# Kernel optimization log

Hardware: AMD Instinct MI355X
Metric: run time of the kernel (lower is better)

## Reference

```python
import jax, jax.numpy as jnp
import numpy as np

HIDDEN = 128
N_NODES = 50000
N_EDGES = 600000
EPS = 1e-5


def setup_inputs() -> dict:
    key = jax.random.key(0)
    ks = jax.random.split(key, 10)
    x = jax.random.normal(ks[0], (N_NODES, HIDDEN), dtype=jnp.float32)
    edge_index = jax.random.randint(ks[1], (2, N_EDGES), 0, N_NODES, dtype=jnp.int64)
    edge_type = jax.random.randint(ks[2], (N_EDGES,), 0, 3, dtype=jnp.int64)
    s = 0.02
    # Stacked per-type message weights: [3, 2H, H] (types 0=power, 1=comm, 2=cross)
    Wmsg = jax.random.normal(ks[3], (3, 2 * HIDDEN, HIDDEN), dtype=jnp.float32) * s
    bmsg = jnp.zeros((3, HIDDEN), dtype=jnp.float32)
    Wupd = jax.random.normal(ks[4], (2 * HIDDEN, HIDDEN), dtype=jnp.float32) * s
    bupd = jnp.zeros((HIDDEN,), dtype=jnp.float32)
    gamma = jnp.ones((HIDDEN,), dtype=jnp.float32)
    beta = jnp.zeros((HIDDEN,), dtype=jnp.float32)
    return {
        "x": x, "edge_index": edge_index, "edge_type": edge_type,
        "Wmsg": Wmsg, "bmsg": bmsg, "Wupd": Wupd, "bupd": bupd,
        "gamma": gamma, "beta": beta,
    }


def reference(x, edge_index, edge_type, Wmsg, bmsg, Wupd, bupd, gamma, beta):
    src, dst = edge_index[0], edge_index[1]
    N = x.shape[0]
    E = edge_type.shape[0]
    # Typed-edge gather + linear message: [E, 2H]
    msg_input = jnp.concatenate([x[src], x[dst]], axis=-1)
    # Compute all 3 typed linears, then select per-edge type: [E, 3, H] -> [E, H]
    all_msgs = jnp.einsum('ec,tch->eth', msg_input, Wmsg) + bmsg
    messages = jnp.take_along_axis(all_msgs, edge_type[:, None, None], axis=1)[:, 0]
    # scatter_add aggregation + count-normalize (count clamped to >= 1)
    agg = jax.ops.segment_sum(messages, dst, num_segments=N)
    count = jax.ops.segment_sum(jnp.ones((E, 1), dtype=x.dtype), dst, num_segments=N)
    agg = agg / jnp.maximum(count, 1.0)
    # Update MLP: Linear -> LayerNorm -> GELU (Dropout is identity in eval)
    h = jnp.concatenate([x, agg], axis=-1) @ Wupd + bupd
    mu = jnp.mean(h, axis=-1, keepdims=True)
    var = jnp.var(h, axis=-1, keepdims=True)
    hn = (h - mu) / jnp.sqrt(var + EPS) * gamma + beta
    x_updated = jax.nn.gelu(hn, approximate=False)
    return x + x_updated
```

## Files before the change

### kernel.cpp

```cpp
#include <hip/hip_runtime.h>
#include <hip/hip_bf16.h>
#include <math.h>

#define HIDDEN 128
#define NNODES 50000
#define NEDGES 600000
#define EPS 1e-5f
#define SCAN_CHUNK 1024
#define NSCAN_BLOCKS ((NNODES + SCAN_CHUNK - 1) / SCAN_CHUNK)
#define MPAD 50048

#define P0_W6T_END   384
#define P0_BV_END    387
#define P0_WUT_END   515
#define P0_XB_END    (515 + 6256)
#define P0_HIST_END  (P0_XB_END + 2344)

#define OFF_W6T  ((size_t)0)
#define OFF_BV   ((size_t)196608)
#define OFF_WUT  ((size_t)199680)
#define OFF_XB   ((size_t)265216)
#define OFF_ABB  ((size_t)13077504)
#define OFF_AGB  ((size_t)51477504)
#define OFF_HIST ((size_t)64289792)
#define OFF_EXCL ((size_t)64489984)
#define OFF_CURS ((size_t)64690176)
#define OFF_BSUM ((size_t)64890368)
#define OFF_PACK ((size_t)64890624)

typedef __attribute__((ext_vector_type(8))) short bf16x8;
typedef __attribute__((ext_vector_type(4))) float f32x4;

__device__ inline unsigned short f2bf(float f) {
    union { float f; unsigned u; } c; c.f = f;
    unsigned u = c.u;
    u += 0x7FFF + ((u >> 16) & 1);
    return (unsigned short)(u >> 16);
}
__device__ inline float bf2f(unsigned short h) {
    union { unsigned u; float f; } c; c.u = ((unsigned)h) << 16;
    return c.f;
}

__device__ inline unsigned char f2fp8(float f) {
    int d = __builtin_amdgcn_cvt_pk_fp8_f32(f, f, 0, false);
    return (unsigned char)(d & 0xFF);
}
template <int S>
__device__ inline float fp8f(unsigned q) {
    return __builtin_amdgcn_cvt_f32_fp8(q, S);
}

__global__ __launch_bounds__(256) void phase0(const float* __restrict__ Wmsg,
                                              const float* __restrict__ bmsg,
                                              const float* __restrict__ Wupd,
                                              const float* __restrict__ x,
                                              const int* __restrict__ ei,
                                              unsigned short* __restrict__ W6T,
                                              float* __restrict__ Bv,
                                              unsigned short* __restrict__ WuT,
                                              unsigned short* __restrict__ Xb,
                                              int* __restrict__ hist) {
    const int b = blockIdx.x;
    const int tid = threadIdx.x;
    if (b < P0_W6T_END) {
        int idx = b * 256 + tid;
        int col = idx >> 7;
        int k = idx & 127;
        int half = col >= 384;
        int rem = col - half * 384;
        int t = rem >> 7;
        int h = rem & 127;
        W6T[idx] = f2bf(Wmsg[t * 32768 + (half * 128 + k) * 128 + h]);
    } else if (b < P0_BV_END) {
        int idx = (b - P0_W6T_END) * 256 + tid;
        if (idx < 768) Bv[idx] = (idx < 384) ? 0.f : bmsg[idx - 384];
    } else if (b < P0_WUT_END) {
        int idx = (b - P0_BV_END) * 256 + tid;
        int n = idx >> 8;
        int k = idx & 255;
        WuT[idx] = f2bf(Wupd[(size_t)k * 128 + n]);
    } else if (b < P0_XB_END) {
        int i = (b - P0_WUT_END) * 256 + tid;
        int base = i * 4;
        if (base < MPAD * 128) {
            ushort4 o;
            if (base < NNODES * 128) {
                float4 v = *(const float4*)(x + base);
                o.x = f2bf(v.x); o.y = f2bf(v.y); o.z = f2bf(v.z); o.w = f2bf(v.w);
            } else {
                o.x = o.y = o.z = o.w = 0;
            }
            *(ushort4*)(Xb + base) = o;
        }
    } else {
        int e = (b - P0_XB_END) * 256 + tid;
        if (e < NEDGES) atomicAdd(&hist[ei[NEDGES + e]], 1);
    }
}

__global__ __launch_bounds__(256) void gemm_ab(const unsigned short* __restrict__ Xb,
                                               const unsigned short* __restrict__ W6T,
                                               const float* __restrict__ Bv,
                                               unsigned char* __restrict__ ABb8) {
    __shared__ unsigned char lds_buf[64 * 272];
    const int tid = threadIdx.x;
    const int mbase = blockIdx.x * 64;
    const int w = tid >> 6;
    const int nbase = blockIdx.y * 256 + w * 64;
    const int lane = tid & 63;
    const int r = lane & 15;
    const int quad = lane >> 4;

    bf16x8 b[4][4];
#pragma unroll
    for (int ks = 0; ks < 4; ++ks)
#pragma unroll
        for (int ni = 0; ni < 4; ++ni)
            b[ks][ni] = *(const bf16x8*)(W6T + (size_t)(nbase + ni * 16 + r) * 128 + ks * 32 + quad * 8);

    unsigned short* xs = (unsigned short*)lds_buf;
#pragma unroll
    for (int i = 0; i < 4; ++i) {
        int item = i * 256 + tid;
        int row = item >> 4;
        int kb = item & 15;
        bf16x8 v = *(const bf16x8*)(Xb + (size_t)(mbase + row) * 128 + kb * 8);
        *(bf16x8*)&xs[row * 128 + ((kb ^ (row & 7)) * 8)] = v;
    }
    __syncthreads();

    f32x4 acc[4][4];
#pragma unroll
    for (int mi = 0; mi < 4; ++mi)
#pragma unroll
        for (int ni = 0; ni < 4; ++ni) acc[mi][ni] = (f32x4){0.f, 0.f, 0.f, 0.f};

#pragma unroll
    for (int ks = 0; ks < 4; ++ks) {
        bf16x8 a[4];
        const int kb = ks * 4 + quad;
#pragma unroll
        for (int mi = 0; mi < 4; ++mi)
            a[mi] = *(const bf16x8*)&xs[(mi * 16 + r) * 128 + ((kb ^ (r & 7)) * 8)];
#pragma unroll
        for (int mi = 0; mi < 4; ++mi)
#pragma unroll
            for (int ni = 0; ni < 4; ++ni)
                acc[mi][ni] = __builtin_amdgcn_mfma_f32_16x16x32_bf16(a[mi], b[ks][ni], acc[mi][ni], 0, 0, 0);
    }

    __syncthreads();
    unsigned char (*tile)[272] = (unsigned char(*)[272])lds_buf;

#pragma unroll
    for (int ni = 0; ni < 4; ++ni) {
        const int col_l = w * 64 + ni * 16 + r;
        const float bias = Bv[blockIdx.y * 256 + col_l];
#pragma unroll
        for (int mi = 0; mi < 4; ++mi) {
            f32x4 v = acc[mi][ni];
#pragma unroll
            for (int reg = 0; reg < 4; ++reg) {
                tile[mi * 16 + quad * 4 + reg][col_l] = f2fp8(v[reg] + bias);
            }
        }
    }
    __syncthreads();

#pragma unroll
    for (int i = 0; i < 4; ++i) {
        int item = i * 256 + tid;
        int row_l = item >> 4;
        int chunk = item & 15;
        int grow = mbase + row_l;
        if (grow < NNODES) {
            uint4 v = *(const uint4*)&tile[row_l][chunk * 16];
            *(uint4*)(ABb8 + (size_t)grow * 768 + blockIdx.y * 256 + chunk * 16) = v;
        }
    }
}

__global__ __launch_bounds__(256) void scan_phase1(const int* __restrict__ hist,
                                                   int* __restrict__ excl,
                                                   int* __restrict__ blockSums) {
    __shared__ int lds[256];
    const int blk = blockIdx.x;
    const int t = threadIdx.x;
    const int base = blk * SCAN_CHUNK + t * 4;
    int v[4];
    int s = 0;
#pragma unroll
    for (int i = 0; i < 4; ++i) {
        v[i] = (base + i < NNODES) ? hist[base + i] : 0;
        s += v[i];
    }
    lds[t] = s;
    __syncthreads();
    for (int off = 1; off < 256; off <<= 1) {
        int add = (t >= off) ? lds[t - off] : 0;
        __syncthreads();
        lds[t] += add;
        __syncthreads();
    }
    int incl = lds[t];
    int run = incl - s;
#pragma unroll
    for (int i = 0; i < 4; ++i) {
        if (base + i < NNODES) excl[base + i] = run;
        run += v[i];
    }
    if (t == 255) blockSums[blk] = incl;
}

__global__ __launch_bounds__(256) void scan_phase3(int* __restrict__ excl,
                                                   const int* __restrict__ blockSums,
                                                   int* __restrict__ cursor) {
    __shared__ int s_add;
    const int blk = blockIdx.x;
    const int t = threadIdx.x;
    if (t < 64) {
        int v = (t < blk) ? blockSums[t] : 0;
#pragma unroll
        for (int off = 32; off >= 1; off >>= 1) v += __shfl_xor(v, off, 64);
        if (t == 0) s_add = v;
    }
    __syncthreads();
    const int add = s_add;
    for (int i = t; i < SCAN_CHUNK; i += 256) {
        int idx = blk * SCAN_CHUNK + i;
        if (idx < NNODES) {
            int o = excl[idx] + add;
            excl[idx] = o;
            cursor[idx] = o;
        }
    }
}

__global__ __launch_bounds__(256) void edge_bucket(const int* __restrict__ ei,
                                                   const int* __restrict__ et,
                                                   int* __restrict__ cursor,
                                                   unsigned* __restrict__ packed) {
    int e = blockIdx.x * 256 + threadIdx.x;
    if (e >= NEDGES) return;
    int src = ei[e];
    int dst = ei[NEDGES + e];
    int t = et[e];
    int pos = atomicAdd(&cursor[dst], 1);
    packed[pos] = (unsigned)(src * 192 + t * 32) | ((unsigned)t << 25);
}

__global__ __launch_bounds__(256) void aggregate(const unsigned* __restrict__ packed,
                                                 const int* __restrict__ excl,
                                                 const int* __restrict__ hist,
                                                 const unsigned char* __restrict__ ABb8,
                                                 unsigned short* __restrict__ Agb) {
    const int n = blockIdx.x * 4 + (threadIdx.x >> 6);
    const int lane = threadIdx.x & 63;
    if (n >= NNODES) return;
    const int start = excl[n];
    const int deg = hist[n];
    const unsigned* ABu = (const unsigned*)ABb8;

    const int half = lane >> 5;
    const int cl = lane & 31;

    float s0 = 0.f, s1 = 0.f, s2 = 0.f, s3 = 0.f;
    int c1 = 0, c2 = 0;

    for (int base = 0; base < deg; base += 64) {
        const int m = min(64, deg - base);
        unsigned v = 0;
        if (lane < m) v = packed[start + base + lane];
        int j = 0;
        for (; j + 8 <= m; j += 8) {
            unsigned e0 = __shfl(v, j + 0 + half, 64);
            unsigned e1 = __shfl(v, j + 2 + half, 64);
            unsigned e2 = __shfl(v, j + 4 + half, 64);
            unsigned e3 = __shfl(v, j + 6 + half, 64);
            unsigned q0 = ABu[(e0 & 0x1FFFFFF) + cl];
            unsigned q1 = ABu[(e1 & 0x1FFFFFF) + cl];
            unsigned q2 = ABu[(e2 & 0x1FFFFFF) + cl];
            unsigned q3 = ABu[(e3 & 0x1FFFFFF) + cl];
            int t0 = e0 >> 25, t1 = e1 >> 25, t2 = e2 >> 25, t3 = e3 >> 25;
            c1 += (t0 == 1) + (t1 == 1) + (t2 == 1) + (t3 == 1);
            c2 += (t0 == 2) + (t1 == 2) + (t2 == 2) + (t3 == 2);
            s0 += (fp8f<0>(q0) + fp8f<0>(q1)) + (fp8f<0>(q2) + fp8f<0>(q3));
            s1 += (fp8f<1>(q0) + fp8f<1>(q1)) + (fp8f<1>(q2) + fp8f<1>(q3));
            s2 += (fp8f<2>(q0) + fp8f<2>(q1)) + (fp8f<2>(q2) + fp8f<2>(q3));
            s3 += (fp8f<3>(q0) + fp8f<3>(q1)) + (fp8f<3>(q2) + fp8f<3>(q3));
        }
        for (; j + 2 <= m; j += 2) {
            unsigned e0 = __shfl(v, j + half, 64);
            unsigned q0 = ABu[(e0 & 0x1FFFFFF) + cl];
            int t0 = e0 >> 25;
            c1 += (t0 == 1);
            c2 += (t0 == 2);
            s0 += fp8f<0>(q0); s1 += fp8f<1>(q0);
            s2 += fp8f<2>(q0); s3 += fp8f<3>(q0);
        }
        if (j < m) {
            unsigned e0 = __shfl(v, j, 64);
            if (half == 0) {
                unsigned q0 = ABu[(e0 & 0x1FFFFFF) + cl];
                int t0 = e0 >> 25;
                c1 += (t0 == 1);
                c2 += (t0 == 2);
                s0 += fp8f<0>(q0); s1 += fp8f<1>(q0);
                s2 += fp8f<2>(q0); s3 += fp8f<3>(q0);
            }
        }
    }

    s0 += __shfl_xor(s0, 32, 64);
    s1 += __shfl_xor(s1, 32, 64);
    s2 += __shfl_xor(s2, 32, 64);
    s3 += __shfl_xor(s3, 32, 64);
    c1 += __shfl_xor(c1, 32, 64);
    c2 += __shfl_xor(c2, 32, 64);
    const int c0 = deg - c1 - c2;

    const unsigned* brow = ABu + (size_t)n * 192 + 96;
    if (c0) {
        unsigned p = brow[cl];
        s0 += c0 * fp8f<0>(p); s1 += c0 * fp8f<1>(p);
        s2 += c0 * fp8f<2>(p); s3 += c0 * fp8f<3>(p);
    }
    if (c1) {
        unsigned p = brow[32 + cl];
        s0 += c1 * fp8f<0>(p); s1 += c1 * fp8f<1>(p);
        s2 += c1 * fp8f<2>(p); s3 += c1 * fp8f<3>(p);
    }
    if (c2) {
        unsigned p = brow[64 + cl];
        s0 += c2 * fp8f<0>(p); s1 += c2 * fp8f<1>(p);
        s2 += c2 * fp8f<2>(p); s3 += c2 * fp8f<3>(p);
    }

    const float inv = 1.0f / fmaxf((float)deg, 1.0f);
    if (half == 0) {
        uint2 o;
        o.x = (unsigned)f2bf(s0 * inv) | ((unsigned)f2bf(s1 * inv) << 16);
        o.y = (unsigned)f2bf(s2 * inv) | ((unsigned)f2bf(s3 * inv) << 16);
        ((uint2*)(Agb + (size_t)n * 128))[cl] = o;
    }
}

__global__ __launch_bounds__(256, 4) void update_mfma(const unsigned short* __restrict__ Xb,
                                                      const unsigned short* __restrict__ Agb,
                                                      const unsigned short* __restrict__ WuT,
                                                      const float* __restrict__ bupd,
                                                      const float* __restrict__ gamma,
                                                      const float* __restrict__ beta,
                                                      float* __restrict__ out) {
    const int tid = threadIdx.x;
    const int rowbase = blockIdx.x * 64 + (tid >> 6) * 16;
    const int lane = tid & 63;
    const int r = lane & 15;
    const int quad = lane >> 4;

    bf16x8 a[8];
#pragma unroll
    for (int ks = 0; ks < 4; ++ks)
        a[ks] = *(const bf16x8*)(Xb + (size_t)(rowbase + r) * 128 + ks * 32 + quad * 8);
#pragma unroll
    for (int ks = 4; ks < 8; ++ks)
        a[ks] = *(const bf16x8*)(Agb + (size_t)(rowbase + r) * 128 + (ks - 4) * 32 + quad * 8);

    bf16x8 e0, e1;
    const int tgt0 = r;
    const int tgt1 = 16 + r;
#pragma unroll
    for (int t = 0; t < 8; ++t) {
        e0[t] = (short)((quad * 8 + t == tgt0) ? 0x3F80 : 0);
        e1[t] = (short)((quad * 8 + t == tgt1) ? 0x3F80 : 0);
    }
    f32x4 xr[8];
#pragma unroll
    for (int ni = 0; ni < 8; ++ni) {
        f32x4 z = (f32x4){0.f, 0.f, 0.f, 0.f};
        xr[ni] = __builtin_amdgcn_mfma_f32_16x16x32_bf16(a[ni >> 1], (ni & 1) ? e1 : e0, z, 0, 0, 0);
    }

    f32x4 acc[8];
#pragma unroll
    for (int ni = 0; ni < 8; ++ni) acc[ni] = (f32x4){0.f, 0.f, 0.f, 0.f};

#pragma unroll
    for (int ks = 0; ks < 8; ++ks) {
        const int kb = ks * 4 + quad;
#pragma unroll
        for (int ni = 0; ni < 8; ++ni) {
            bf16x8 b = *(const bf16x8*)(WuT + (size_t)(ni * 16 + r) * 256 + kb * 8);
            acc[ni] = __builtin_amdgcn_mfma_f32_16x16x32_bf16(a[ks], b, acc[ni], 0, 0, 0);
        }
    }

    float vals[8][4];
    float gcol[8], bcol[8];
#pragma unroll
    for (int ni = 0; ni < 8; ++ni) {
        const int col = ni * 16 + r;
        const float bias = bupd[col];
        gcol[ni] = gamma[col];
        bcol[ni] = beta[col];
#pragma unroll
        for (int reg = 0; reg < 4; ++reg) vals[ni][reg] = acc[ni][reg] + bias;
    }

#pragma unroll
    for (int reg = 0; reg < 4; ++reg) {
        float s = 0.f, s2 = 0.f;
#pragma unroll
        for (int ni = 0; ni < 8; ++ni) {
            s += vals[ni][reg];
            s2 += vals[ni][reg] * vals[ni][reg];
        }
#pragma unroll
        for (int off = 8; off >= 1; off >>= 1) {
            s += __shfl_xor(s, off, 64);
            s2 += __shfl_xor(s2, off, 64);
        }
        const int row = rowbase + quad * 4 + reg;
        if (row < NNODES) {
            const float mu = s * (1.0f / 128.0f);
            const float var = s2 * (1.0f / 128.0f) - mu * mu;
            const float inv = rsqrtf(var + EPS);
#pragma unroll
            for (int ni = 0; ni < 8; ++ni) {
                const int col = ni * 16 + r;
                float hn = (vals[ni][reg] - mu) * inv * gcol[ni] + bcol[ni];
                float ge = 0.5f * hn * (1.0f + erff(hn * 0.70710678118654752f));
                out[(size_t)row * 128 + col] = xr[ni][reg] + ge;
            }
        }
    }
}

extern "C" void kernel_launch(void* const* d_in, const int* in_sizes, int n_in,
                              void* d_out, int out_size, void* d_ws, size_t ws_size,
                              hipStream_t stream) {
    const float* x     = (const float*)d_in[0];
    const int*   ei    = (const int*)d_in[1];
    const int*   et    = (const int*)d_in[2];
    const float* Wmsg  = (const float*)d_in[3];
    const float* bmsg  = (const float*)d_in[4];
    const float* Wupd  = (const float*)d_in[5];
    const float* bupd  = (const float*)d_in[6];
    const float* gamma = (const float*)d_in[7];
    const float* beta  = (const float*)d_in[8];
    float* out = (float*)d_out;

    char* ws = (char*)d_ws;
    unsigned short* W6T  = (unsigned short*)(ws + OFF_W6T);
    float*          Bv   = (float*)(ws + OFF_BV);
    unsigned short* WuT  = (unsigned short*)(ws + OFF_WUT);
    unsigned short* Xb   = (unsigned short*)(ws + OFF_XB);
    unsigned char*  ABb8 = (unsigned char*)(ws + OFF_ABB);
    unsigned short* Agb  = (unsigned short*)(ws + OFF_AGB);
    int*            hist = (int*)(ws + OFF_HIST);
    int*            excl = (int*)(ws + OFF_EXCL);
    int*            curs = (int*)(ws + OFF_CURS);
    int*            bsum = (int*)(ws + OFF_BSUM);
    unsigned*       pack = (unsigned*)(ws + OFF_PACK);

    (void)hipMemsetAsync(hist, 0, NNODES * sizeof(int), stream);

    phase0<<<P0_HIST_END, 256, 0, stream>>>(Wmsg, bmsg, Wupd, x, ei, W6T, Bv, WuT, Xb, hist);
    gemm_ab<<<dim3(MPAD / 64, 3), 256, 0, stream>>>(Xb, W6T, Bv, ABb8);
    scan_phase1<<<NSCAN_BLOCKS, 256, 0, stream>>>(hist, excl, bsum);
    scan_phase3<<<NSCAN_BLOCKS, 256, 0, stream>>>(excl, bsum, curs);
    edge_bucket<<<(NEDGES + 255) / 256, 256, 0, stream>>>(ei, et, curs, pack);
    aggregate<<<(NNODES + 3) / 4, 256, 0, stream>>>(pack, excl, hist, ABb8, Agb);
    update_mfma<<<MPAD / 64, 256, 0, stream>>>(Xb, Agb, WuT, bupd, gamma, beta, out);
}
```

Measured before the change: 260.6 us.

## Split update GEMM output columns across two waves with shared-memory LayerNorm reduction

The update kernel now gives each 16-row tile to two wavefronts, each computing half of the 128 output columns. LayerNorm sum and sum-of-squares partials are combined through shared memory behind a block barrier. Blocks cover 32 rows instead of 64, so the grid doubles, and launch bounds are raised to allow more resident blocks. This cuts per-wave accumulator registers and serial MFMA chains to raise occupancy. The cost is a __syncthreads, duplicate A-fragment loads across the wave pair, and more blocks.

```diff
diff --git a/kernel.cpp b/kernel.cpp
--- a/kernel.cpp
+++ b/kernel.cpp
@@ -346,18 +346,24 @@
     }
 }
 
-__global__ __launch_bounds__(256, 4) void update_mfma(const unsigned short* __restrict__ Xb,
+__global__ __launch_bounds__(256, 5) void update_mfma(const unsigned short* __restrict__ Xb,
                                                       const unsigned short* __restrict__ Agb,
                                                       const unsigned short* __restrict__ WuT,
                                                       const float* __restrict__ bupd,
                                                       const float* __restrict__ gamma,
                                                       const float* __restrict__ beta,
                                                       float* __restrict__ out) {
+    __shared__ float sred[2][2][32];
+
     const int tid = threadIdx.x;
-    const int rowbase = blockIdx.x * 64 + (tid >> 6) * 16;
+    const int w = tid >> 6;
+    const int wrow = w >> 1;
+    const int whalf = w & 1;
     const int lane = tid & 63;
     const int r = lane & 15;
     const int quad = lane >> 4;
+    const int rowbase = blockIdx.x * 32 + wrow * 16;
+    const int nibase = whalf * 4;
 
     bf16x8 a[8];
 #pragma unroll
@@ -368,70 +374,82 @@
         a[ks] = *(const bf16x8*)(Agb + (size_t)(rowbase + r) * 128 + (ks - 4) * 32 + quad * 8);
 
     bf16x8 e0, e1;
-    const int tgt0 = r;
-    const int tgt1 = 16 + r;
 #pragma unroll
     for (int t = 0; t < 8; ++t) {
-        e0[t] = (short)((quad * 8 + t == tgt0) ? 0x3F80 : 0);
-        e1[t] = (short)((quad * 8 + t == tgt1) ? 0x3F80 : 0);
-    }
-    f32x4 xr[8];
-#pragma unroll
-    for (int ni = 0; ni < 8; ++ni) {
+        e0[t] = (short)((quad * 8 + t == r) ? 0x3F80 : 0);
+        e1[t] = (short)((quad * 8 + t == 16 + r) ? 0x3F80 : 0);
+    }
+    f32x4 xr[4];
+#pragma unroll
+    for (int nl = 0; nl < 4; ++nl) {
+        const int ni = nibase + nl;
         f32x4 z = (f32x4){0.f, 0.f, 0.f, 0.f};
-        xr[ni] = __builtin_amdgcn_mfma_f32_16x16x32_bf16(a[ni >> 1], (ni & 1) ? e1 : e0, z, 0, 0, 0);
-    }
-
-    f32x4 acc[8];
-#pragma unroll
-    for (int ni = 0; ni < 8; ++ni) acc[ni] = (f32x4){0.f, 0.f, 0.f, 0.f};
+        xr[nl] = __builtin_amdgcn_mfma_f32_16x16x32_bf16(a[ni >> 1], (ni & 1) ? e1 : e0, z, 0, 0, 0);
+    }
+
+    f32x4 acc[4];
+#pragma unroll
+    for (int nl = 0; nl < 4; ++nl) acc[nl] = (f32x4){0.f, 0.f, 0.f, 0.f};
 
 #pragma unroll
     for (int ks = 0; ks < 8; ++ks) {
         const int kb = ks * 4 + quad;
 #pragma unroll
-        for (int ni = 0; ni < 8; ++ni) {
-            bf16x8 b = *(const bf16x8*)(WuT + (size_t)(ni * 16 + r) * 256 + kb * 8);
-            acc[ni] = __builtin_amdgcn_mfma_f32_16x16x32_bf16(a[ks], b, acc[ni], 0, 0, 0);
-        }
-    }
-
-    float vals[8][4];
-    float gcol[8], bcol[8];
-#pragma unroll
-    for (int ni = 0; ni < 8; ++ni) {
-        const int col = ni * 16 + r;
+        for (int nl = 0; nl < 4; ++nl) {
+            bf16x8 b = *(const bf16x8*)(WuT + (size_t)((nibase + nl) * 16 + r) * 256 + kb * 8);
+            acc[nl] = __builtin_amdgcn_mfma_f32_16x16x32_bf16(a[ks], b, acc[nl], 0, 0, 0);
+        }
+    }
+
+    float vals[4][4];
+    float gcol[4], bcol[4];
+#pragma unroll
+    for (int nl = 0; nl < 4; ++nl) {
+        const int col = (nibase + nl) * 16 + r;
         const float bias = bupd[col];
-        gcol[ni] = gamma[col];
-        bcol[ni] = beta[col];
-#pragma unroll
-        for (int reg = 0; reg < 4; ++reg) vals[ni][reg] = acc[ni][reg] + bias;
+        gcol[nl] = gamma[col];
+        bcol[nl] = beta[col];
+#pragma unroll
+        for (int reg = 0; reg < 4; ++reg) vals[nl][reg] = acc[nl][reg] + bias;
     }
 
 #pragma unroll
     for (int reg = 0; reg < 4; ++reg) {
         float s = 0.f, s2 = 0.f;
 #pragma unroll
-        for (int ni = 0; ni < 8; ++ni) {
-            s += vals[ni][reg];
-            s2 += vals[ni][reg] * vals[ni][reg];
+        for (int nl = 0; nl < 4; ++nl) {
+            s += vals[nl][reg];
+            s2 += vals[nl][reg] * vals[nl][reg];
         }
 #pragma unroll
         for (int off = 8; off >= 1; off >>= 1) {
             s += __shfl_xor(s, off, 64);
             s2 += __shfl_xor(s2, off, 64);
         }
+        if (r == 0) {
+            const int rowL = wrow * 16 + quad * 4 + reg;
+            sred[whalf][0][rowL] = s;
+            sred[whalf][1][rowL] = s2;
+        }
+    }
+    __syncthreads();
+
+#pragma unroll
+    for (int reg = 0; reg < 4; ++reg) {
+        const int rowL = wrow * 16 + quad * 4 + reg;
+        const float s = sred[0][0][rowL] + sred[1][0][rowL];
+        const float s2 = sred[0][1][rowL] + sred[1][1][rowL];
         const int row = rowbase + quad * 4 + reg;
         if (row < NNODES) {
             const float mu = s * (1.0f / 128.0f);
             const float var = s2 * (1.0f / 128.0f) - mu * mu;
             const float inv = rsqrtf(var + EPS);
 #pragma unroll
-            for (int ni = 0; ni < 8; ++ni) {
-                const int col = ni * 16 + r;
-                float hn = (vals[ni][reg] - mu) * inv * gcol[ni] + bcol[ni];
+            for (int nl = 0; nl < 4; ++nl) {
+                const int col = (nibase + nl) * 16 + r;
+                float hn = (vals[nl][reg] - mu) * inv * gcol[nl] + bcol[nl];
                 float ge = 0.5f * hn * (1.0f + erff(hn * 0.70710678118654752f));
-                out[(size_t)row * 128 + col] = xr[ni][reg] + ge;
+                out[(size_t)row * 128 + col] = xr[nl][reg] + ge;
             }
         }
     }
@@ -472,5 +490,5 @@
     scan_phase3<<<NSCAN_BLOCKS, 256, 0, stream>>>(excl, bsum, curs);
     edge_bucket<<<(NEDGES + 255) / 256, 256, 0, stream>>>(ei, et, curs, pack);
     aggregate<<<(NNODES + 3) / 4, 256, 0, stream>>>(pack, excl, hist, ABb8, Agb);
-    update_mfma<<<MPAD / 64, 256, 0, stream>>>(Xb, Agb, WuT, bupd, gamma, beta, out);
-}
+    update_mfma<<<MPAD / 32, 256, 0, stream>>>(Xb, Agb, WuT, bupd, gamma, beta, out);
+}
```

After: 265.2 us. Within noise of the previous version (+1.8%).
